# Kernel optimization log

Measured on AMD Instinct MI355X. Metric: run time of the kernel, lower is better.

The kernel has to match this reference:

```python
import jax, jax.numpy as jnp
import numpy as np

N, E = 100000, 1600000
DIM, H, D = 64, 4, 8          # dim, num_heads, qk_dim
DH = D * H                    # 32
QK_SCALE = (DIM // H) ** -0.5


def setup_inputs() -> dict:
    key = jax.random.key(0)
    k1, k2, k3, k4 = jax.random.split(key, 4)
    x = jax.random.normal(k1, (N, DIM), dtype=jnp.float32)
    edge_index = jax.random.randint(k2, (2, E), 0, N, dtype=jnp.int64)
    W_qkv = jax.random.normal(k3, (DIM, 2 * DH + DIM), dtype=jnp.float32) * (DIM ** -0.5)
    b_qkv = jax.random.normal(k4, (2 * DH + DIM,), dtype=jnp.float32) * 0.02
    return {"x": x, "edge_index": edge_index, "W_qkv": W_qkv, "b_qkv": b_qkv}


def reference(x, edge_index, W_qkv, b_qkv):
    n = x.shape[0]
    e = edge_index.shape[1]
    qkv = x @ W_qkv + b_qkv                       # (N, 2*DH+DIM)
    q = qkv[:, :DH].reshape(n, H, D)
    k = qkv[:, DH:2 * DH].reshape(n, H, D)
    v = qkv[:, 2 * DH:].reshape(n, H, DIM // H)
    s, t = edge_index[0], edge_index[1]
    q_e = q[s] * QK_SCALE                         # (E, H, D)
    k_e = k[t]
    v_e = v[t]                                    # (E, H, DIM/H)
    # scale q by 1/sqrt(num source neighbors) (bincount of s)
    deg = jax.ops.segment_sum(jnp.ones((e,), x.dtype), s, num_segments=n)
    q_e = q_e * (deg[s] ** -0.5)[:, None, None]
    compat = jnp.einsum('ehd,ehd->eh', q_e, k_e)  # (E, H)
    # segment softmax over edges grouped by source node s
    m = jax.ops.segment_max(compat, s, num_segments=n)
    ex = jnp.exp(compat - m[s])
    denom = jax.ops.segment_sum(ex, s, num_segments=n)
    attn = ex / (denom[s] + 1e-16)                # (E, H)
    msg = (v_e * attn[..., None]).reshape(e, DIM)  # (E, DIM)
    out = jax.ops.segment_sum(msg, s, num_segments=n)  # (N, DIM)
    return out
```

## Files before the change

kernel.cpp:

```cpp
#include <hip/hip_runtime.h>


#define NDIM 64
#define NBMAX 1024
#define CTILE 8192
#define STGMAX 4352

static __device__ __forceinline__ unsigned short f2bf(float f) {
    unsigned int u = __float_as_uint(f);
    unsigned int r = (u + 0x7fffu + ((u >> 16) & 1u)) >> 16;
    return (unsigned short)r;
}

__global__ void bucket_count_kernel(const int* __restrict__ s_arr,
                                    unsigned int* __restrict__ bcnt, int E) {
    __shared__ unsigned int h[NBMAX];
    for (int i = threadIdx.x; i < NBMAX; i += blockDim.x) h[i] = 0;
    __syncthreads();
    int i0 = blockIdx.x * blockDim.x + threadIdx.x;
    int st = gridDim.x * blockDim.x;
    for (int e = i0; e < E; e += st)
        atomicAdd(&h[(unsigned)s_arr[e] >> 7], 1u);
    __syncthreads();
    for (int i = threadIdx.x; i < NBMAX; i += blockDim.x)
        if (h[i]) atomicAdd(&bcnt[i], h[i]);
}

__global__ void scan_buckets_kernel(const unsigned int* __restrict__ bcnt,
                                    unsigned int* __restrict__ bbase,
                                    unsigned int* __restrict__ gcur) {
    __shared__ unsigned int sh[1024];
    int tid = threadIdx.x;
    unsigned int v = bcnt[tid];
    unsigned int acc = v;
    sh[tid] = acc;
    __syncthreads();
    for (int off = 1; off < 1024; off <<= 1) {
        unsigned int add = (tid >= off) ? sh[tid - off] : 0;
        __syncthreads();
        acc += add;
        sh[tid] = acc;
        __syncthreads();
    }
    bbase[tid] = acc - v;
    gcur[tid]  = acc - v;
}

__global__ void __launch_bounds__(1024, 2)
bin_kernel(const int* __restrict__ s_arr,
           const int* __restrict__ t_arr,
           unsigned int* __restrict__ gcur,
           unsigned int* __restrict__ binned, int E) {
    __shared__ unsigned int hist[NBMAX];
    __shared__ unsigned int off[NBMAX];
    __shared__ unsigned int gbase[NBMAX];
    __shared__ unsigned int stg[CTILE];
    __shared__ unsigned int psum[NBMAX];
    int tid = threadIdx.x;
    int e0 = blockIdx.x * CTILE;
    int cnt = min(CTILE, E - e0);

    hist[tid] = 0;
    __syncthreads();
    for (int i = tid; i < cnt; i += 1024)
        atomicAdd(&hist[(unsigned)s_arr[e0 + i] >> 7], 1u);
    __syncthreads();

    unsigned int v = hist[tid];
    unsigned int acc = v;
    psum[tid] = acc;
    __syncthreads();
    for (int o = 1; o < 1024; o <<= 1) {
        unsigned int add = (tid >= o) ? psum[tid - o] : 0;
        __syncthreads();
        acc += add;
        psum[tid] = acc;
        __syncthreads();
    }
    off[tid] = acc - v;
    __syncthreads();

    for (int i = tid; i < cnt; i += 1024) {
        int s = s_arr[e0 + i];
        int t = t_arr[e0 + i];
        unsigned int bkt = (unsigned)s >> 7;
        unsigned int p = atomicAdd(&off[bkt], 1u);
        stg[p] = ((unsigned)(s & 127) << 17) | (unsigned)t;
    }
    __syncthreads();

    {
        unsigned int h = hist[tid];
        gbase[tid] = h ? atomicAdd(&gcur[tid], h) : 0u;
    }
    __syncthreads();

    int wid = tid >> 6, lane = tid & 63;
    for (int b = wid; b < NBMAX; b += 16) {
        unsigned int h = hist[b];
        if (h == 0) continue;
        unsigned int src = off[b] - h;
        unsigned int dst = gbase[b];
        for (unsigned int i = lane; i < h; i += 64)
            binned[dst + i] = stg[src + i];
    }
}

__global__ void qkv_gemm_kernel(const float* __restrict__ x,
                                const float* __restrict__ W,
                                const float* __restrict__ b,
                                float* __restrict__ qs,
                                unsigned short* __restrict__ kv, int N) {
    int col = threadIdx.x & 127;
    int rw  = threadIdx.x >> 7;
    float w[64];
    #pragma unroll
    for (int k = 0; k < 64; ++k) w[k] = W[k * 128 + col];
    float bias = b[col];
    __shared__ float4 xs[8][16];

    for (int r0 = blockIdx.x * 8; r0 < N; r0 += gridDim.x * 8) {
        __syncthreads();
        if (threadIdx.x < 128) {
            int rr = threadIdx.x >> 4;
            int cc = threadIdx.x & 15;
            int n = r0 + rr;
            xs[rr][cc] = (n < N)
                ? reinterpret_cast<const float4*>(x)[(size_t)n * 16 + cc]
                : make_float4(0.f, 0.f, 0.f, 0.f);
        }
        __syncthreads();
        #pragma unroll
        for (int rsub = 0; rsub < 4; ++rsub) {
            int rr = rw * 4 + rsub;
            int n = r0 + rr;
            if (n < N) {
                float acc = bias;
                #pragma unroll
                for (int k4 = 0; k4 < 16; ++k4) {
                    float4 xv = xs[rr][k4];
                    acc = fmaf(xv.x, w[4 * k4 + 0], acc);
                    acc = fmaf(xv.y, w[4 * k4 + 1], acc);
                    acc = fmaf(xv.z, w[4 * k4 + 2], acc);
                    acc = fmaf(xv.w, w[4 * k4 + 3], acc);
                }
                if (col < 32) {
                    qs[(size_t)n * 32 + col] = acc;
                } else if (col < 64) {
                    kv[(size_t)n * 96 + (col - 32)] = f2bf(acc);
                } else {
                    kv[(size_t)n * 96 + 32 + (col - 64)] = f2bf(acc);
                }
            }
        }
    }
}

__global__ void __launch_bounds__(1024, 2)
sort_aggregate_kernel(const unsigned int* __restrict__ bbase,
                      const unsigned int* __restrict__ bcnt,
                      const unsigned int* __restrict__ binned,
                      const float* __restrict__ qs,
                      const unsigned int* __restrict__ kv32,
                      float* __restrict__ out, int N) {
    __shared__ unsigned int hist[128];
    __shared__ unsigned int rstart[128];
    __shared__ unsigned int cur[128];
    __shared__ unsigned int sh[128];
    __shared__ unsigned int stg[STGMAX];

    int b = blockIdx.x;
    int tid = threadIdx.x;
    unsigned int base = bbase[b];
    unsigned int cnt = min(bcnt[b], (unsigned int)STGMAX);

    if (tid < 128) hist[tid] = 0;
    __syncthreads();
    for (unsigned int i = tid; i < cnt; i += 1024)
        atomicAdd(&hist[binned[base + i] >> 17], 1u);
    __syncthreads();

    unsigned int v = (tid < 128) ? hist[tid] : 0;
    unsigned int acc = v;
    if (tid < 128) sh[tid] = acc;
    __syncthreads();
    for (int o = 1; o < 128; o <<= 1) {
        unsigned int add = (tid >= o && tid < 128) ? sh[tid - o] : 0;
        __syncthreads();
        if (tid < 128) { acc += add; sh[tid] = acc; }
        __syncthreads();
    }
    if (tid < 128) {
        unsigned int exc = acc - v;
        rstart[tid] = exc;
        cur[tid] = exc;
    }
    __syncthreads();

    for (unsigned int i = tid; i < cnt; i += 1024) {
        unsigned int e = binned[base + i];
        unsigned int p = atomicAdd(&cur[e >> 17], 1u);
        stg[p] = e & 0x1FFFFu;
    }
    __syncthreads();

    int wid = tid >> 6, lane = tid & 63;
    unsigned int ulane = (unsigned int)lane;
    int csrc = (lane < 16) ? (lane & ~3)
             : (lane < 48) ? (((lane - 16) >> 3) << 2)
                           : 0;

    for (int nl = wid * 8; nl < wid * 8 + 8; ++nl) {
        int n = b * 128 + nl;
        if (n >= N) break;
        int dg = (int)hist[nl];
        if (dg == 0) {
            if (lane >= 16 && lane < 48)
                *reinterpret_cast<float2*>(&out[(size_t)n * 64 + 2 * (lane - 16)]) =
                    make_float2(0.f, 0.f);
            continue;
        }
        int start = (int)rstart[nl];
        int end = start + dg;
        float sc = 0.25f * rsqrtf((float)dg);
        float q0 = 0.f, q1 = 0.f;
        if (lane < 16) {
            q0 = qs[(size_t)n * 32 + 2 * lane] * sc;
            q1 = qs[(size_t)n * 32 + 2 * lane + 1] * sc;
        }

        float accx = 0.f, accy = 0.f, den = 0.f;
        int j = start;
        for (; j + 7 < end; j += 8) {
            unsigned int t[8], r[8];
            #pragma unroll
            for (int i = 0; i < 8; ++i) t[i] = stg[j + i];
            #pragma unroll
            for (int i = 0; i < 8; ++i)
                r[i] = (lane < 48) ? kv32[t[i] * 48u + ulane] : 0u;
            float lo[8], hi[8], p[8];
            #pragma unroll
            for (int i = 0; i < 8; ++i) {
                lo[i] = __uint_as_float(r[i] << 16);
                hi[i] = __uint_as_float(r[i] & 0xffff0000u);
                p[i] = fmaf(q0, lo[i], q1 * hi[i]);
            }
            #pragma unroll
            for (int i = 0; i < 8; ++i) {
                p[i] += __shfl_xor(p[i], 1);
                p[i] += __shfl_xor(p[i], 2);
            }
            #pragma unroll
            for (int i = 0; i < 8; ++i) {
                float c = __shfl(p[i], csrc);
                float w = __expf(c);
                accx = fmaf(w, lo[i], accx);
                accy = fmaf(w, hi[i], accy);
                den += w;
            }
        }
        for (; j + 3 < end; j += 4) {
            unsigned int t[4], r[4];
            #pragma unroll
            for (int i = 0; i < 4; ++i) t[i] = stg[j + i];
            #pragma unroll
            for (int i = 0; i < 4; ++i)
                r[i] = (lane < 48) ? kv32[t[i] * 48u + ulane] : 0u;
            #pragma unroll
            for (int i = 0; i < 4; ++i) {
                float lo = __uint_as_float(r[i] << 16);
                float hi = __uint_as_float(r[i] & 0xffff0000u);
                float p = fmaf(q0, lo, q1 * hi);
                p += __shfl_xor(p, 1);
                p += __shfl_xor(p, 2);
                float c = __shfl(p, csrc);
                float w = __expf(c);
                accx = fmaf(w, lo, accx);
                accy = fmaf(w, hi, accy);
                den += w;
            }
        }
        for (; j < end; ++j) {
            unsigned int t0 = stg[j];
            unsigned int r0 = (lane < 48) ? kv32[t0 * 48u + ulane] : 0u;
            float lo = __uint_as_float(r0 << 16);
            float hi = __uint_as_float(r0 & 0xffff0000u);
            float p = fmaf(q0, lo, q1 * hi);
            p += __shfl_xor(p, 1);
            p += __shfl_xor(p, 2);
            float c = __shfl(p, csrc);
            float w = __expf(c);
            accx = fmaf(w, lo, accx);
            accy = fmaf(w, hi, accy);
            den += w;
        }
        if (lane >= 16 && lane < 48) {
            float inv = 1.0f / (den + 1e-16f);
            float2 o = make_float2(accx * inv, accy * inv);
            *reinterpret_cast<float2*>(&out[(size_t)n * 64 + 2 * (lane - 16)]) = o;
        }
    }
}

extern "C" void kernel_launch(void* const* d_in, const int* in_sizes, int n_in,
                              void* d_out, int out_size, void* d_ws, size_t ws_size,
                              hipStream_t stream) {
    const float* x = (const float*)d_in[0];
    const int*   eidx = (const int*)d_in[1];
    const float* W = (const float*)d_in[2];
    const float* b = (const float*)d_in[3];
    int N = in_sizes[0] / NDIM;
    int E = in_sizes[1] / 2;
    float* out = (float*)d_out;

    int NB = (N + 127) / 128;

    float* qs = (float*)d_ws;
    unsigned short* kv = (unsigned short*)(qs + (size_t)N * 32);
    unsigned int* bcnt  = (unsigned int*)(kv + (size_t)N * 96);
    unsigned int* bbase = bcnt + NBMAX;
    unsigned int* gcur  = bbase + NBMAX;
    unsigned int* binned = gcur + NBMAX;

    const int* s_arr = eidx;
    const int* t_arr = eidx + E;

    hipMemsetAsync(bcnt, 0, NBMAX * sizeof(unsigned int), stream);

    bucket_count_kernel<<<512, 256, 0, stream>>>(s_arr, bcnt, E);
    scan_buckets_kernel<<<1, 1024, 0, stream>>>(bcnt, bbase, gcur);
    bin_kernel<<<(E + CTILE - 1) / CTILE, 1024, 0, stream>>>(s_arr, t_arr, gcur, binned, E);
    qkv_gemm_kernel<<<2048, 256, 0, stream>>>(x, W, b, qs, kv, N);
    sort_aggregate_kernel<<<NB, 1024, 0, stream>>>(
        bbase, bcnt, binned, qs, (const unsigned int*)kv, out, N);
}
```

Before: 177.0 us.

## Halve aggregate block size and software-pipeline neighbor KV gathers

```diff
diff --git a/kernel.cpp b/kernel.cpp
--- a/kernel.cpp
+++ b/kernel.cpp
@@ -156,7 +156,21 @@
     }
 }
 
-__global__ void __launch_bounds__(1024, 2)
+#define COMPUTE_EDGE(rr)                                              \
+    {                                                                 \
+        float lo = __uint_as_float((rr) << 16);                       \
+        float hi = __uint_as_float((rr) & 0xffff0000u);               \
+        float p = fmaf(q0, lo, q1 * hi);                              \
+        p += __shfl_xor(p, 1);                                        \
+        p += __shfl_xor(p, 2);                                        \
+        float c = __shfl(p, csrc);                                    \
+        float w = __expf(c);                                          \
+        accx = fmaf(w, lo, accx);                                     \
+        accy = fmaf(w, hi, accy);                                     \
+        den += w;                                                     \
+    }
+
+__global__ void __launch_bounds__(512, 8)
 sort_aggregate_kernel(const unsigned int* __restrict__ bbase,
                       const unsigned int* __restrict__ bcnt,
                       const unsigned int* __restrict__ binned,
@@ -176,7 +190,7 @@
 
     if (tid < 128) hist[tid] = 0;
     __syncthreads();
-    for (unsigned int i = tid; i < cnt; i += 1024)
+    for (unsigned int i = tid; i < cnt; i += 512)
         atomicAdd(&hist[binned[base + i] >> 17], 1u);
     __syncthreads();
 
@@ -197,20 +211,22 @@
     }
     __syncthreads();
 
-    for (unsigned int i = tid; i < cnt; i += 1024) {
+    for (unsigned int i = tid; i < cnt; i += 512) {
         unsigned int e = binned[base + i];
         unsigned int p = atomicAdd(&cur[e >> 17], 1u);
-        stg[p] = e & 0x1FFFFu;
+        stg[p] = (e & 0x1FFFFu) * 192u;
     }
     __syncthreads();
 
     int wid = tid >> 6, lane = tid & 63;
-    unsigned int ulane = (unsigned int)lane;
+    unsigned int lane4 = ((unsigned int)lane) << 2;
+    bool ldact = (lane < 48);
+    const char* kvb = (const char*)kv32;
     int csrc = (lane < 16) ? (lane & ~3)
              : (lane < 48) ? (((lane - 16) >> 3) << 2)
                            : 0;
 
-    for (int nl = wid * 8; nl < wid * 8 + 8; ++nl) {
+    for (int nl = wid * 16; nl < wid * 16 + 16; ++nl) {
         int n = b * 128 + nl;
         if (n >= N) break;
         int dg = (int)hist[nl];
@@ -221,7 +237,6 @@
             continue;
         }
         int start = (int)rstart[nl];
-        int end = start + dg;
         float sc = 0.25f * rsqrtf((float)dg);
         float q0 = 0.f, q1 = 0.f;
         if (lane < 16) {
@@ -231,69 +246,44 @@
 
         float accx = 0.f, accy = 0.f, den = 0.f;
         int j = start;
-        for (; j + 7 < end; j += 8) {
-            unsigned int t[8], r[8];
-            #pragma unroll
-            for (int i = 0; i < 8; ++i) t[i] = stg[j + i];
-            #pragma unroll
-            for (int i = 0; i < 8; ++i)
-                r[i] = (lane < 48) ? kv32[t[i] * 48u + ulane] : 0u;
-            float lo[8], hi[8], p[8];
-            #pragma unroll
-            for (int i = 0; i < 8; ++i) {
-                lo[i] = __uint_as_float(r[i] << 16);
-                hi[i] = __uint_as_float(r[i] & 0xffff0000u);
-                p[i] = fmaf(q0, lo[i], q1 * hi[i]);
+        int rem = dg;
+
+        unsigned int ra0 = 0, ra1 = 0, ra2 = 0, ra3 = 0;
+        if (rem >= 4) {
+            unsigned int o0 = stg[j] + lane4,     o1 = stg[j + 1] + lane4;
+            unsigned int o2 = stg[j + 2] + lane4, o3 = stg[j + 3] + lane4;
+            if (ldact) {
+                ra0 = *(const unsigned int*)(kvb + o0);
+                ra1 = *(const unsigned int*)(kvb + o1);
+                ra2 = *(const unsigned int*)(kvb + o2);
+                ra3 = *(const unsigned int*)(kvb + o3);
             }
-            #pragma unroll
-            for (int i = 0; i < 8; ++i) {
-                p[i] += __shfl_xor(p[i], 1);
-                p[i] += __shfl_xor(p[i], 2);
+        }
+        while (rem >= 4) {
+            unsigned int rb0 = 0, rb1 = 0, rb2 = 0, rb3 = 0;
+            if (rem >= 8) {
+                unsigned int o0 = stg[j + 4] + lane4, o1 = stg[j + 5] + lane4;
+                unsigned int o2 = stg[j + 6] + lane4, o3 = stg[j + 7] + lane4;
+                if (ldact) {
+                    rb0 = *(const unsigned int*)(kvb + o0);
+                    rb1 = *(const unsigned int*)(kvb + o1);
+                    rb2 = *(const unsigned int*)(kvb + o2);
+                    rb3 = *(const unsigned int*)(kvb + o3);
+                }
             }
-            #pragma unroll
-            for (int i = 0; i < 8; ++i) {
-                float c = __shfl(p[i], csrc);
-                float w = __expf(c);
-                accx = fmaf(w, lo[i], accx);
-                accy = fmaf(w, hi[i], accy);
-                den += w;
-            }
-        }
-        for (; j + 3 < end; j += 4) {
-            unsigned int t[4], r[4];
-            #pragma unroll
-            for (int i = 0; i < 4; ++i) t[i] = stg[j + i];
-            #pragma unroll
-            for (int i = 0; i < 4; ++i)
-                r[i] = (lane < 48) ? kv32[t[i] * 48u + ulane] : 0u;
-            #pragma unroll
-            for (int i = 0; i < 4; ++i) {
-                float lo = __uint_as_float(r[i] << 16);
-                float hi = __uint_as_float(r[i] & 0xffff0000u);
-                float p = fmaf(q0, lo, q1 * hi);
-                p += __shfl_xor(p, 1);
-                p += __shfl_xor(p, 2);
-                float c = __shfl(p, csrc);
-                float w = __expf(c);
-                accx = fmaf(w, lo, accx);
-                accy = fmaf(w, hi, accy);
-                den += w;
-            }
-        }
-        for (; j < end; ++j) {
-            unsigned int t0 = stg[j];
-            unsigned int r0 = (lane < 48) ? kv32[t0 * 48u + ulane] : 0u;
-            float lo = __uint_as_float(r0 << 16);
-            float hi = __uint_as_float(r0 & 0xffff0000u);
-            float p = fmaf(q0, lo, q1 * hi);
-            p += __shfl_xor(p, 1);
-            p += __shfl_xor(p, 2);
-            float c = __shfl(p, csrc);
-            float w = __expf(c);
-            accx = fmaf(w, lo, accx);
-            accy = fmaf(w, hi, accy);
-            den += w;
-        }
+            COMPUTE_EDGE(ra0);
+            COMPUTE_EDGE(ra1);
+            COMPUTE_EDGE(ra2);
+            COMPUTE_EDGE(ra3);
+            ra0 = rb0; ra1 = rb1; ra2 = rb2; ra3 = rb3;
+            j += 4; rem -= 4;
+        }
+        for (; rem > 0; --rem, ++j) {
+            unsigned int o0 = stg[j] + lane4;
+            unsigned int r0 = ldact ? *(const unsigned int*)(kvb + o0) : 0u;
+            COMPUTE_EDGE(r0);
+        }
+
         if (lane >= 16 && lane < 48) {
             float inv = 1.0f / (den + 1e-16f);
             float2 o = make_float2(accx * inv, accy * inv);
@@ -331,6 +321,6 @@
     scan_buckets_kernel<<<1, 1024, 0, stream>>>(bcnt, bbase, gcur);
     bin_kernel<<<(E + CTILE - 1) / CTILE, 1024, 0, stream>>>(s_arr, t_arr, gcur, binned, E);
     qkv_gemm_kernel<<<2048, 256, 0, stream>>>(x, W, b, qs, kv, N);
-    sort_aggregate_kernel<<<NB, 1024, 0, stream>>>(
+    sort_aggregate_kernel<<<NB, 512, 0, stream>>>(
         bbase, bcnt, binned, qs, (const unsigned int*)kv, out, N);
 }
```

After: 178.3 us. Within noise of the previous version (+0.7%).
